# Optimization experiments

Measured on AMD Instinct MI355X. Metric: run time of the kernel, lower is better.

The kernel has to match this reference:

```python
import jax, jax.numpy as jnp
import numpy as np

H = 16            # num_heads
SEG = 2048        # segment_size
DIL = 8           # dilation_rate
BLOCK_M = 64      # triton query block size (min(64, M_padded))


def setup_inputs() -> dict:
    key = jax.random.key(0)
    k1, k2, k3 = jax.random.split(key, 3)
    B, M, D = 2, 8192, 1024
    x = jax.random.normal(k1, (B, M, D), dtype=jnp.float32)
    Wqkv = jax.random.normal(k2, (3 * D, D), dtype=jnp.float32) * 0.02
    Wout = jax.random.normal(k3, (D, D), dtype=jnp.float32) * 0.02
    return {"x": x, "Wqkv": Wqkv, "Wout": Wout}


def reference(x, Wqkv, Wout):
    B, M, D = x.shape
    hd = D // H
    scale = hd ** -0.5
    S = M // SEG                      # number of segments (M is a multiple of SEG)
    Kn = SEG // DIL                   # dilated keys per segment
    nb = SEG // BLOCK_M               # query blocks per segment

    # qkv projection (torch Linear: x @ W^T), split into q,k,v: [B,H,M,hd]
    qkv = jnp.einsum('bmd,ed->bme', x, Wqkv).reshape(B, M, 3, H, hd)
    qkv = jnp.transpose(qkv, (2, 0, 3, 1, 4))
    q, k, v = qkv[0] * scale, qkv[1], qkv[2]

    # segment-local views
    q4 = q.reshape(B, H, S, SEG, hd)
    k4 = k.reshape(B, H, S, SEG, hd)[:, :, :, ::DIL]   # [B,H,S,Kn,hd] dilated keys
    v4 = v.reshape(B, H, S, SEG, hd)[:, :, :, ::DIL]

    # scores per segment: [B,H,S,SEG,Kn]
    scores = jnp.einsum('bhspd,bhskd->bhspk', q4, k4)
    # kernel normalization: per key j, subtract max over the 64-query block
    scores = scores.reshape(B, H, S, nb, BLOCK_M, Kn)
    c = jnp.max(scores, axis=4, keepdims=True)          # [B,H,S,nb,1,Kn]
    w = jnp.exp(scores - c)
    den = jnp.sum(w, axis=-1) + 1e-10                   # [B,H,S,nb,BLOCK_M]
    num = jnp.einsum('bhsnmk,bhskd->bhsnmd', w, v4)
    out = num / den[..., None]                          # [B,H,S,nb,BLOCK_M,hd]

    out = out.reshape(B, H, M, hd)
    out = jnp.transpose(out, (0, 2, 1, 3)).reshape(B, M, D)
    return jnp.einsum('bmd,ed->bme', out, Wout)
```

## Files before the change

kernel.cpp:

```cpp
#include <hip/hip_runtime.h>
#include <hip/hip_bf16.h>
#include <stdint.h>


typedef __attribute__((ext_vector_type(8))) short short8;
typedef __attribute__((ext_vector_type(4))) float f32x4;
typedef __attribute__((ext_vector_type(4))) unsigned short ushort4v;

#define DEVI static __device__ __forceinline__

DEVI unsigned short f2bf(float f) {
  union { float f; uint32_t u; } v; v.f = f;
  return (unsigned short)((v.u + 0x7FFFu + ((v.u >> 16) & 1u)) >> 16);
}

DEVI uint32_t pack_bf16(float lo, float hi) {
  return (uint32_t)f2bf(lo) | ((uint32_t)f2bf(hi) << 16);
}

DEVI void gload_lds16(const void* g, void* l) {
  __builtin_amdgcn_global_load_lds((const __attribute__((address_space(1))) void*)g,
                                   (__attribute__((address_space(3))) void*)l,
                                   16, 0, 0);
}

__global__ void cvt_kernel(const float* __restrict__ in, unsigned short* __restrict__ out, int n) {
  int i = (blockIdx.x * 256 + threadIdx.x) * 4;
  if (i >= n) return;
  float4 f = *(const float4*)(in + i);
  uint2 o;
  o.x = (uint32_t)f2bf(f.x) | ((uint32_t)f2bf(f.y) << 16);
  o.y = (uint32_t)f2bf(f.z) | ((uint32_t)f2bf(f.w) << 16);
  *(uint2*)(out + i) = o;
}

template<int EPI>
__global__ __launch_bounds__(256, 2) void gemm_bt(
    const unsigned short* __restrict__ A, const unsigned short* __restrict__ B,
    void* __restrict__ Cv, unsigned short* __restrict__ Cv2,
    float scale, long a_row_stride, int ldc, int K)
{
  __shared__ unsigned short smA[128 * 64];
  __shared__ unsigned short smB[128 * 64];
  const int tid = threadIdx.x;
  const int tm = blockIdx.x, tn = blockIdx.y;
  const int w = tid >> 6, lane = tid & 63;
  const int wr = (w >> 1) * 64, wc = (w & 1) * 64;
  const int lr = lane & 15, lq = lane >> 4;

  int se[4], srow[4], scol[4];
#pragma unroll
  for (int i = 0; i < 4; ++i) {
    int e = (i * 256 + tid) * 8;
    int r = e >> 6;
    int cc = (e >> 3) & 7;
    se[i] = e; srow[i] = r; scol[i] = (cc ^ (r & 7)) * 8;
  }

  f32x4 acc[4][4] = {};

  for (int kt = 0; kt < K / 64; ++kt) {
    if (kt) __syncthreads();
#pragma unroll
    for (int i = 0; i < 4; ++i)
      gload_lds16(A + (long)(tm * 128 + srow[i]) * a_row_stride + kt * 64 + scol[i], &smA[se[i]]);
#pragma unroll
    for (int i = 0; i < 4; ++i)
      gload_lds16(B + (long)(tn * 128 + srow[i]) * K + kt * 64 + scol[i], &smB[se[i]]);
    __syncthreads();

#pragma unroll
    for (int kk = 0; kk < 2; ++kk) {
      int kc = kk * 4 + lq;
      short8 af[4], bfm[4];
#pragma unroll
      for (int i = 0; i < 4; ++i) {
        int row = wr + i * 16 + lr;
        af[i] = *(const short8*)&smA[row * 64 + ((kc ^ (row & 7)) * 8)];
      }
#pragma unroll
      for (int j = 0; j < 4; ++j) {
        int row = wc + j * 16 + lr;
        bfm[j] = *(const short8*)&smB[row * 64 + ((kc ^ (row & 7)) * 8)];
      }
#pragma unroll
      for (int i = 0; i < 4; ++i)
#pragma unroll
        for (int j = 0; j < 4; ++j)
          acc[i][j] = __builtin_amdgcn_mfma_f32_16x16x32_bf16(af[i], bfm[j], acc[i][j], 0, 0, 0);
    }
  }

  if (EPI == 2 && tn >= 8) {
    const int fbase = (tn - 8) * 128 + wc;
#pragma unroll
    for (int ip = 0; ip < 4; ip += 2) {
      int t0 = tm * 128 + wr + ip * 16 + lq * 4;
      int seg = t0 >> 8;
      int ts  = t0 & 255;
      int c32 = (ts >> 5) * 16 + (ts & 15);
#pragma unroll
      for (int j = 0; j < 4; ++j) {
        int f = fbase + j * 16 + lr;
        uint32_t* rp = (uint32_t*)&Cv2[((long)(seg * 1024 + f)) * 256];
        uint4 U;
        U.x = pack_bf16(acc[ip][j][0] * scale, acc[ip + 1][j][0] * scale);
        U.y = pack_bf16(acc[ip][j][1] * scale, acc[ip + 1][j][1] * scale);
        U.z = pack_bf16(acc[ip][j][2] * scale, acc[ip + 1][j][2] * scale);
        U.w = pack_bf16(acc[ip][j][3] * scale, acc[ip + 1][j][3] * scale);
        *(uint4*)&rp[c32] = U;
      }
    }
    return;
  }

#pragma unroll
  for (int i = 0; i < 4; ++i) {
    int rg0 = tm * 128 + wr + i * 16 + lq * 4;
#pragma unroll
    for (int j = 0; j < 4; ++j) {
      int cg = tn * 128 + wc + j * 16 + lr;
#pragma unroll
      for (int r = 0; r < 4; ++r) {
        float v = acc[i][j][r] * scale;
        long off = (long)(rg0 + r) * ldc + cg;
        if (EPI == 0) ((float*)Cv)[off] = v;
        else          ((unsigned short*)Cv)[off] = f2bf(v);
      }
    }
  }
}

__global__ __launch_bounds__(256, 2) void attn_kernel(
    const unsigned short* __restrict__ qb,
    const unsigned short* __restrict__ kb,
    const unsigned short* __restrict__ vtb,
    unsigned short* __restrict__ attout)
{
  __shared__ unsigned short v_t[64 * 256];
  __shared__ uint32_t w32[4][64][18];

  const int u = (blockIdx.x & 7) * 128 + (blockIdx.x >> 3);
  const int e8 = u & 7, h = (u >> 3) & 15, s = (u >> 7) & 3, b = u >> 9;
  const int tid = threadIdx.x, w = tid >> 6, lane = tid & 63;
  const int lr = lane & 15, lq = lane >> 4;
  const long qrow0 = (long)b * 8192 + s * 2048 + e8 * 256 + w * 64;
  const int hc = h * 64;

  const unsigned short* kbase = kb + ((long)(b * 4 + s) * 256) * 1024 + hc;
  const unsigned short* vbase = vtb + ((long)(b * 4 + s) * 1024 + hc) * 256;

#pragma unroll
  for (int it = 0; it < 8; ++it) {
    int e = (it * 256 + tid) * 8;
    int f = e >> 8;
    int ch = (e >> 3) & 31;
    gload_lds16(vbase + (long)f * 256 + ((ch ^ (f & 7)) * 8), &v_t[e]);
  }

  const unsigned short* qbase = qb + qrow0 * 1024 + hc;
  short8 aq[4][2];
#pragma unroll
  for (int i = 0; i < 4; ++i)
#pragma unroll
    for (int kk = 0; kk < 2; ++kk)
      aq[i][kk] = *(const short8*)&qbase[(i * 16 + lr) * 1024 + (kk * 4 + lq) * 8];

  __syncthreads();

  short8 ones;
#pragma unroll
  for (int e = 0; e < 8; ++e) ones[e] = (short)0x3F80;

  uint32_t (*wsl)[18] = w32[w];

  f32x4 acc_pv[4][4] = {};
  f32x4 acc_den[4] = {};

  short8 bkc[2][2], bkn[2][2];
#pragma unroll
  for (int j = 0; j < 2; ++j)
#pragma unroll
    for (int kk = 0; kk < 2; ++kk)
      bkc[j][kk] = *(const short8*)&kbase[(long)(j * 16 + lr) * 1024 + (kk * 4 + lq) * 8];

#pragma unroll
  for (int c = 0; c < 8; ++c) {
    if (c < 7) {
#pragma unroll
      for (int j = 0; j < 2; ++j)
#pragma unroll
        for (int kk = 0; kk < 2; ++kk)
          bkn[j][kk] = *(const short8*)
            &kbase[(long)((c + 1) * 32 + j * 16 + lr) * 1024 + (kk * 4 + lq) * 8];
    }

    f32x4 acc_s[4][2] = {};
#pragma unroll
    for (int kk = 0; kk < 2; ++kk)
#pragma unroll
      for (int i = 0; i < 4; ++i)
#pragma unroll
        for (int j = 0; j < 2; ++j)
          acc_s[i][j] = __builtin_amdgcn_mfma_f32_16x16x32_bf16(aq[i][kk], bkc[j][kk], acc_s[i][j], 0, 0, 0);

    float cmax[2];
#pragma unroll
    for (int j = 0; j < 2; ++j) {
      float m = -3.4e38f;
#pragma unroll
      for (int i = 0; i < 4; ++i)
#pragma unroll
        for (int r = 0; r < 4; ++r) m = fmaxf(m, acc_s[i][j][r]);
      m = fmaxf(m, __shfl_xor(m, 16));
      m = fmaxf(m, __shfl_xor(m, 32));
      cmax[j] = m;
    }

#pragma unroll
    for (int i = 0; i < 4; ++i) {
#pragma unroll
      for (int r = 0; r < 4; ++r) {
        int q = i * 16 + lq * 4 + r;
        wsl[q][lr] = pack_bf16(__expf(acc_s[i][0][r] - cmax[0]),
                               __expf(acc_s[i][1][r] - cmax[1]));
      }
    }

    short8 av[4];
#pragma unroll
    for (int ct = 0; ct < 4; ++ct) {
      int frow = ct * 16 + lr;
      av[ct] = *(const short8*)&v_t[frow * 256 + (((c * 4 + lq) ^ (frow & 7)) << 3)];
    }
#pragma unroll
    for (int qi = 0; qi < 4; ++qi) {
      short8 bw = *(const short8*)&wsl[qi * 16 + lr][lq * 4];
      acc_den[qi] = __builtin_amdgcn_mfma_f32_16x16x32_bf16(ones, bw, acc_den[qi], 0, 0, 0);
#pragma unroll
      for (int ct = 0; ct < 4; ++ct)
        acc_pv[qi][ct] = __builtin_amdgcn_mfma_f32_16x16x32_bf16(av[ct], bw, acc_pv[qi][ct], 0, 0, 0);
    }

#pragma unroll
    for (int j = 0; j < 2; ++j)
#pragma unroll
      for (int kk = 0; kk < 2; ++kk)
        bkc[j][kk] = bkn[j][kk];
  }

#pragma unroll
  for (int qi = 0; qi < 4; ++qi) {
    float inv = 1.0f / (acc_den[qi][0] + 1e-10f);
    long orow = (qrow0 + qi * 16 + lr) * 1024 + hc;
#pragma unroll
    for (int ct = 0; ct < 4; ++ct) {
      ushort4v p;
#pragma unroll
      for (int r = 0; r < 4; ++r) p[r] = f2bf(acc_pv[qi][ct][r] * inv);
      *(ushort4v*)&attout[orow + ct * 16 + lq * 4] = p;
    }
  }
}

extern "C" void kernel_launch(void* const* d_in, const int* in_sizes, int n_in,
                              void* d_out, int out_size, void* d_ws, size_t ws_size,
                              hipStream_t stream) {
  (void)in_sizes; (void)n_in; (void)out_size; (void)ws_size;
  const float* x    = (const float*)d_in[0];
  const float* Wqkv = (const float*)d_in[1];
  const float* Wout = (const float*)d_in[2];
  float* out = (float*)d_out;
  char* ws = (char*)d_ws;

  unsigned short* xb     = (unsigned short*)(ws);
  unsigned short* attout = (unsigned short*)(ws);
  unsigned short* wqkvb  = (unsigned short*)(ws + 33554432);
  unsigned short* woutb  = (unsigned short*)(ws + 39845888);
  unsigned short* qbuf   = (unsigned short*)(ws + 41943040);
  unsigned short* kbuf   = (unsigned short*)(ws + 75497472);
  unsigned short* vtb    = (unsigned short*)(ws + 79691776);

  cvt_kernel<<<16384, 256, 0, stream>>>(x, xb, 16777216);
  cvt_kernel<<<3072, 256, 0, stream>>>(Wqkv, wqkvb, 3 * 1024 * 1024);
  cvt_kernel<<<1024, 256, 0, stream>>>(Wout, woutb, 1024 * 1024);

  gemm_bt<1><<<dim3(128, 8), 256, 0, stream>>>(
      xb, wqkvb, (void*)qbuf, nullptr, 0.125f, 1024, 1024, 1024);
  gemm_bt<2><<<dim3(16, 16), 256, 0, stream>>>(
      xb, wqkvb + 1024 * 1024, (void*)kbuf, vtb, 1.0f, 8192, 1024, 1024);

  attn_kernel<<<1024, 256, 0, stream>>>(qbuf, kbuf, vtb, attout);

  gemm_bt<0><<<dim3(128, 8), 256, 0, stream>>>(
      attout, woutb, (void*)out, nullptr, 1.0f, 1024, 1024, 1024);
}
```

Before: 184.1 us.

## Add 256x256 eight-wave pipelined GEMM for Q and output projections

Adds a new GEMM kernel with 256x256 tiles, 512 threads, and double-buffered LDS fed by direct global-to-LDS loads. Loads for the next k-tile are interleaved across eight MFMA phases with fine-grained vmcnt waits and s_setprio. It replaces the 128x128 gemm_bt for the Q projection and the output projection. The goal is better data reuse and hiding of memory latency. In exchange it uses 128KB of LDS and large accumulators per thread, which may limit occupancy, and it hardcodes K=1024.

After: 172.1 us. 6.5% less time.

```diff
diff --git a/kernel.cpp b/kernel.cpp
--- a/kernel.cpp
+++ b/kernel.cpp
@@ -32,6 +32,124 @@
   o.x = (uint32_t)f2bf(f.x) | ((uint32_t)f2bf(f.y) << 16);
   o.y = (uint32_t)f2bf(f.z) | ((uint32_t)f2bf(f.w) << 16);
   *(uint2*)(out + i) = o;
+}
+
+#define STAGE_A(bf, hf, kt) do { \
+  gload_lds16(Abase + (long)((hf) * 128 + srow0) * 1024 + (kt) * 64 + scol0, &smA[bf][hf][se0]); \
+  gload_lds16(Abase + (long)((hf) * 128 + srow1) * 1024 + (kt) * 64 + scol1, &smA[bf][hf][se1]); \
+} while (0)
+#define STAGE_B(bf, hf, kt) do { \
+  gload_lds16(Bbase + (long)((hf) * 128 + srow0) * 1024 + (kt) * 64 + scol0, &smB[bf][hf][se0]); \
+  gload_lds16(Bbase + (long)((hf) * 128 + srow1) * 1024 + (kt) * 64 + scol1, &smB[bf][hf][se1]); \
+} while (0)
+
+template<bool OUT_F32>
+__global__ __launch_bounds__(512, 2) void gemm8p(
+    const unsigned short* __restrict__ A, const unsigned short* __restrict__ B,
+    void* __restrict__ Cv, float scale)
+{
+  __shared__ unsigned short smA[2][2][128 * 64];
+  __shared__ unsigned short smB[2][2][128 * 64];
+  const int tid = threadIdx.x;
+  const int tm = blockIdx.x, tn = blockIdx.y;
+  const int w = tid >> 6, lane = tid & 63;
+  const int wm = w >> 2, wn = w & 3;
+  const int lr = lane & 15, lq = lane >> 4;
+
+  const int e0 = tid * 8,        e1 = (512 + tid) * 8;
+  const int srow0 = e0 >> 6,     srow1 = e1 >> 6;
+  const int sc0 = (e0 >> 3) & 7, sc1 = (e1 >> 3) & 7;
+  const int scol0 = (sc0 ^ (srow0 & 7)) * 8, scol1 = (sc1 ^ (srow1 & 7)) * 8;
+  const int se0 = e0, se1 = e1;
+
+  const unsigned short* Abase = A + (long)tm * 256 * 1024;
+  const unsigned short* Bbase = B + (long)tn * 256 * 1024;
+
+  f32x4 acc[8][4] = {};
+
+  STAGE_A(0, 0, 0); STAGE_B(0, 0, 0); STAGE_A(0, 1, 0); STAGE_B(0, 1, 0);
+  asm volatile("s_waitcnt vmcnt(4)" ::: "memory");
+  __builtin_amdgcn_s_barrier();
+  asm volatile("" ::: "memory");
+
+  for (int t = 0; t < 8; ++t) {
+#pragma unroll
+    for (int p = 0; p < 8; ++p) {
+      const int o = p >> 2;
+      const int a = p & 1;
+      const int b = (p >> 1) & 1;
+
+      short8 af[4][2], bfr[2][2];
+#pragma unroll
+      for (int mi2 = 0; mi2 < 4; ++mi2) {
+        int r = wm * 64 + mi2 * 16 + lr;
+#pragma unroll
+        for (int kk = 0; kk < 2; ++kk) {
+          int kc = kk * 4 + lq;
+          af[mi2][kk] = *(const short8*)&smA[o][a][r * 64 + ((kc ^ (r & 7)) * 8)];
+        }
+      }
+#pragma unroll
+      for (int nj2 = 0; nj2 < 2; ++nj2) {
+        int r = wn * 32 + nj2 * 16 + lr;
+#pragma unroll
+        for (int kk = 0; kk < 2; ++kk) {
+          int kc = kk * 4 + lq;
+          bfr[nj2][kk] = *(const short8*)&smB[o][b][r * 64 + ((kc ^ (r & 7)) * 8)];
+        }
+      }
+
+      switch (p) {
+        case 0: STAGE_A(1, 0, 2 * t + 1); break;
+        case 1: STAGE_B(1, 0, 2 * t + 1); break;
+        case 2: STAGE_A(1, 1, 2 * t + 1); break;
+        case 3: STAGE_B(1, 1, 2 * t + 1); break;
+        case 4: if (t < 7) STAGE_A(0, 0, 2 * t + 2); break;
+        case 5: if (t < 7) STAGE_B(0, 0, 2 * t + 2); break;
+        case 6: if (t < 7) STAGE_A(0, 1, 2 * t + 2); break;
+        case 7: if (t < 7) STAGE_B(0, 1, 2 * t + 2); break;
+      }
+
+      __builtin_amdgcn_s_setprio(1);
+#pragma unroll
+      for (int kk = 0; kk < 2; ++kk)
+#pragma unroll
+        for (int mi2 = 0; mi2 < 4; ++mi2)
+#pragma unroll
+          for (int nj2 = 0; nj2 < 2; ++nj2)
+            acc[a * 4 + mi2][b * 2 + nj2] = __builtin_amdgcn_mfma_f32_16x16x32_bf16(
+                af[mi2][kk], bfr[nj2][kk], acc[a * 4 + mi2][b * 2 + nj2], 0, 0, 0);
+      __builtin_amdgcn_s_setprio(0);
+
+      if (t < 7) {
+        asm volatile("s_waitcnt vmcnt(4)" ::: "memory");
+      } else {
+        if (p < 4)       asm volatile("s_waitcnt vmcnt(4)" ::: "memory");
+        else if (p == 4) asm volatile("s_waitcnt vmcnt(2)" ::: "memory");
+        else             asm volatile("s_waitcnt vmcnt(0)" ::: "memory");
+      }
+      __builtin_amdgcn_s_barrier();
+      asm volatile("" ::: "memory");
+    }
+  }
+
+  const int row0 = tm * 256 + wm * 64 + lq * 4;
+  const int col0 = tn * 256 + wn * 32 + lr;
+#pragma unroll
+  for (int mi = 0; mi < 8; ++mi) {
+    int row = row0 + (mi & 3) * 16 + (mi >> 2) * 128;
+#pragma unroll
+    for (int nj = 0; nj < 4; ++nj) {
+      int col = col0 + (nj & 1) * 16 + (nj >> 1) * 128;
+#pragma unroll
+      for (int rr = 0; rr < 4; ++rr) {
+        float v = acc[mi][nj][rr] * scale;
+        long off = (long)(row + rr) * 1024 + col;
+        if (OUT_F32) ((float*)Cv)[off] = v;
+        else         ((unsigned short*)Cv)[off] = f2bf(v);
+      }
+    }
+  }
 }
 
 template<int EPI>
@@ -285,13 +403,11 @@
   cvt_kernel<<<3072, 256, 0, stream>>>(Wqkv, wqkvb, 3 * 1024 * 1024);
   cvt_kernel<<<1024, 256, 0, stream>>>(Wout, woutb, 1024 * 1024);
 
-  gemm_bt<1><<<dim3(128, 8), 256, 0, stream>>>(
-      xb, wqkvb, (void*)qbuf, nullptr, 0.125f, 1024, 1024, 1024);
+  gemm8p<false><<<dim3(64, 4), 512, 0, stream>>>(xb, wqkvb, (void*)qbuf, 0.125f);
   gemm_bt<2><<<dim3(16, 16), 256, 0, stream>>>(
       xb, wqkvb + 1024 * 1024, (void*)kbuf, vtb, 1.0f, 8192, 1024, 1024);
 
   attn_kernel<<<1024, 256, 0, stream>>>(qbuf, kbuf, vtb, attout);
 
-  gemm_bt<0><<<dim3(128, 8), 256, 0, stream>>>(
-      attout, woutb, (void*)out, nullptr, 1.0f, 1024, 1024, 1024);
-}
+  gemm8p<true><<<dim3(64, 4), 512, 0, stream>>>(attout, woutb, (void*)out, 1.0f);
+}
```
